# Kernel tuning notes

Measured on AMD Instinct MI355X. Metric: run time of the kernel, lower is better.

Reference implementation:

```python
import jax, jax.numpy as jnp
import numpy as np

WS = 16          # window_size
NUM_HEADS = 6

def _rel_tables(ws):
    # SwinV2 continuous relative coords table, log-spaced, scaled by 8
    r = np.arange(-(ws - 1), ws, dtype=np.float32)
    t = np.stack(np.meshgrid(r, r, indexing='ij'), axis=-1)      # (2ws-1, 2ws-1, 2)
    t = t / (ws - 1) * 8.0
    t = np.sign(t) * np.log2(np.abs(t) + 1.0) / np.log2(8.0)
    c = np.stack(np.meshgrid(np.arange(ws), np.arange(ws), indexing='ij')).reshape(2, -1)
    rel = (c[:, :, None] - c[:, None, :]).transpose(1, 2, 0)     # (N, N, 2)
    rel[..., 0] += ws - 1
    rel[..., 1] += ws - 1
    rel[..., 0] *= 2 * ws - 1
    return jnp.asarray(t), jnp.asarray(rel.sum(-1))              # table, (N,N) int index

REL_TABLE, REL_INDEX = _rel_tables(WS)

def conv2d(x, w, b, pad=0, dil=1, groups=1):
    y = jax.lax.conv_general_dilated(
        x, w, (1, 1), [(pad, pad), (pad, pad)], rhs_dilation=(dil, dil),
        feature_group_count=groups, dimension_numbers=('NCHW', 'OIHW', 'NCHW'))
    return y + b[None, :, None, None]

def layernorm(x, g, b, eps=1e-5):
    mu = x.mean(-1, keepdims=True)
    var = ((x - mu) ** 2).mean(-1, keepdims=True)
    return (x - mu) * jax.lax.rsqrt(var + eps) * g + b

def _forward(x, p1_w, p1_b, pw_w, pw_b, dw_w, dw_b, dd_w, dd_b, p2_w, p2_b,
             ln_g, ln_b, qkv_w, q_bias, v_bias, logit_scale,
             cpb_w1, cpb_b1, cpb_w2, proj_w, proj_b):
    B, C, H, W = x.shape
    ws, nh = WS, NUM_HEADS
    N, hd = ws * ws, C // nh
    # ---- VAB: conv attention block ----
    y = jax.nn.gelu(conv2d(x, p1_w, p1_b), approximate=False)          # proj_1 + GELU
    a = conv2d(y, pw_w, pw_b)                                          # pointwise 1x1
    a = conv2d(a, dw_w, dw_b, pad=2, groups=C)                         # depthwise 5x5
    a = conv2d(a, dd_w, dd_b, pad=6, dil=3, groups=C)                  # depthwise 5x5 dil=3
    y = conv2d(y * a, p2_w, p2_b) + x                                  # proj_2 + residual
    y = jnp.transpose(y, (0, 2, 3, 1))                                 # B,H,W,C
    y = layernorm(y, ln_g, ln_b)                                       # pixel_norm
    # ---- window partition -> (B*nW, N, C) ----
    xw = y.reshape(B, H // ws, ws, W // ws, ws, C)
    xw = xw.transpose(0, 1, 3, 2, 4, 5).reshape(-1, N, C)
    # ---- SwinV2 cosine window attention ----
    qkv_b = jnp.concatenate([q_bias, jnp.zeros_like(v_bias), v_bias])
    qkv = (xw @ qkv_w.T + qkv_b).reshape(-1, N, 3, nh, hd).transpose(2, 0, 3, 1, 4)
    q, k, v = qkv[0], qkv[1], qkv[2]                                   # (B_, h, N, d)
    qn = q / jnp.maximum(jnp.linalg.norm(q, axis=-1, keepdims=True), 1e-12)
    kn = k / jnp.maximum(jnp.linalg.norm(k, axis=-1, keepdims=True), 1e-12)
    scale = jnp.exp(jnp.minimum(logit_scale, jnp.log(100.0)))          # clamp at 1/0.01
    attn = jnp.einsum('bhnd,bhmd->bhnm', qn, kn) * scale
    # CPB MLP bias: (2ws-1,2ws-1,2) -> heads, gathered by relative_position_index
    t = (jax.nn.relu(REL_TABLE @ cpb_w1.T + cpb_b1) @ cpb_w2.T).reshape(-1, nh)
    rpb = t[REL_INDEX.reshape(-1)].reshape(N, N, nh).transpose(2, 0, 1)
    attn = attn + 16.0 * jax.nn.sigmoid(rpb)
    attn = jax.nn.softmax(attn, axis=-1)
    out = jnp.einsum('bhnm,bhmd->bhnd', attn, v).transpose(0, 2, 1, 3).reshape(-1, N, C)
    out = out @ proj_w.T + proj_b
    # ---- window reverse -> NCHW ----
    out = out.reshape(B, H // ws, W // ws, ws, ws, C)
    out = out.transpose(0, 1, 3, 2, 4, 5).reshape(B, H, W, C)
    return jnp.transpose(out, (0, 3, 1, 2))

def setup_inputs():
    key = jax.random.key(0)
    ks = jax.random.split(key, 12)
    C, A = 192, 192
    rn = lambda k, shape, s=0.02: jax.random.normal(k, shape, jnp.float32) * s
    return {
        'x': jax.random.normal(ks[0], (4, C, 128, 128), jnp.float32),
        'p1_w': rn(ks[1], (A, C, 1, 1)), 'p1_b': jnp.zeros((A,), jnp.float32),
        'pw_w': rn(ks[2], (A, A, 1, 1)), 'pw_b': jnp.zeros((A,), jnp.float32),
        'dw_w': rn(ks[3], (A, 1, 5, 5), 0.05), 'dw_b': jnp.zeros((A,), jnp.float32),
        'dd_w': rn(ks[4], (A, 1, 5, 5), 0.05), 'dd_b': jnp.zeros((A,), jnp.float32),
        'p2_w': rn(ks[5], (C, A, 1, 1)), 'p2_b': jnp.zeros((C,), jnp.float32),
        'ln_g': jnp.ones((C,), jnp.float32), 'ln_b': jnp.zeros((C,), jnp.float32),
        'qkv_w': rn(ks[6], (3 * C, C)),
        'q_bias': jnp.zeros((C,), jnp.float32), 'v_bias': jnp.zeros((C,), jnp.float32),
        'logit_scale': jnp.log(10.0) * jnp.ones((NUM_HEADS, 1, 1), jnp.float32),
        'cpb_w1': rn(ks[7], (512, 2), 0.1), 'cpb_b1': jnp.zeros((512,), jnp.float32),
        'cpb_w2': rn(ks[8], (NUM_HEADS, 512), 0.1),
        'proj_w': rn(ks[9], (C, C)), 'proj_b': jnp.zeros((C,), jnp.float32),
    }

def reference(x, p1_w, p1_b, pw_w, pw_b, dw_w, dw_b, dd_w, dd_b, p2_w, p2_b,
              ln_g, ln_b, qkv_w, q_bias, v_bias, logit_scale,
              cpb_w1, cpb_b1, cpb_w2, proj_w, proj_b):
    return _forward(x, p1_w, p1_b, pw_w, pw_b, dw_w, dw_b, dd_w, dd_b, p2_w, p2_b,
                    ln_g, ln_b, qkv_w, q_bias, v_bias, logit_scale,
                    cpb_w1, cpb_b1, cpb_w2, proj_w, proj_b)
```

## Files before the change

### kernel.cpp

```cpp
#include <hip/hip_runtime.h>
#include <hip/hip_bf16.h>
#include <math.h>

#define HWC 16384
#define CCH 192
#define LDA 200

typedef __attribute__((ext_vector_type(8))) short short8x;
typedef __attribute__((ext_vector_type(4))) float f32x4;

__device__ __forceinline__ float b2f(unsigned int u){
  union { unsigned int i; float f; } x; x.i = (u & 0xffffu) << 16; return x.f;
}
__device__ __forceinline__ unsigned short f2b(float f){
  union { float f; unsigned int i; } x; x.f = f;
  unsigned int r = x.i + 0x7FFFu + ((x.i >> 16) & 1u);
  return (unsigned short)(r >> 16);
}
__device__ __forceinline__ unsigned int cvt_pk_bf16(float a, float b){
  unsigned int r;
  asm("v_cvt_pk_bf16_f32 %0, %1, %2" : "=v"(r) : "v"(a), "v"(b));
  return r;
}
__device__ __forceinline__ float exp2_fast(float x){
  float r;
  asm("v_exp_f32 %0, %1" : "=v"(r) : "v"(x));
  return r;
}
__device__ __forceinline__ float gelu_exact(float v){
  return 0.5f * v * (1.0f + erff(v * 0.70710678118654752440f));
}

__global__ __launch_bounds__(256) void cast_w_kernel(
    const float* __restrict__ qkvw, const float* __restrict__ projw,
    const float* __restrict__ p1w,  const float* __restrict__ pww,
    const float* __restrict__ p2w,  const float* __restrict__ dww,
    const float* __restrict__ ddw,
    unsigned short* __restrict__ wq,  unsigned short* __restrict__ wprj,
    unsigned short* __restrict__ wp1, unsigned short* __restrict__ wpa,
    unsigned short* __restrict__ wp2, float* __restrict__ dwt,
    float* __restrict__ ddt)
{
  int i = blockIdx.x*256 + threadIdx.x;
  if (i < 110592) wq[i] = f2b(qkvw[i]);
  if (i < 36864){
    wprj[i] = f2b(projw[i]);
    wp1[i]  = f2b(p1w[i]);
    wpa[i]  = f2b(pww[i]);
    wp2[i]  = f2b(p2w[i]);
  }
  if (i < 4992){
    int t = i / 192, c = i - t*192;
    dwt[i] = (t < 25) ? dww[c*25 + t] : 0.0f;
    ddt[i] = (t < 25) ? ddw[c*25 + t] : 0.0f;
  }
}

__global__ __launch_bounds__(256) void tx_kernel(
    const float* __restrict__ in, float* __restrict__ xt32,
    unsigned short* __restrict__ x16)
{
  __shared__ float xs[CCH*68];
  const int tid = threadIdx.x;
  const int pix0 = blockIdx.x * 64;
  const int bb = pix0 >> 14;
  const int hw0 = pix0 & (HWC-1);
  const long base = (long)bb * CCH * HWC + hw0;
  #pragma unroll 8
  for (int i=0;i<48;i++){
    int idx = tid + i*256;
    int ci = idx >> 6, pix = idx & 63;
    xs[ci*68 + pix] = in[base + (long)ci*HWC + pix];
  }
  __syncthreads();
  #pragma unroll 8
  for (int i=0;i<48;i++){
    int idx = tid + i*256;
    int pix = idx / 192, ci = idx - pix*192;
    float v = xs[ci*68 + pix];
    long g = (long)(pix0 + pix)*CCH + ci;
    xt32[g] = v;
    x16[g]  = f2b(v);
  }
}

__global__ __launch_bounds__(256, 3) void pw01_mfma(
    const unsigned short* __restrict__ x16,
    const unsigned short* __restrict__ w1,
    const float* __restrict__ b1,
    const unsigned short* __restrict__ wa,
    const float* __restrict__ ba,
    unsigned short* __restrict__ y16,
    unsigned short* __restrict__ a16)
{
  __shared__ unsigned short sA[128*LDA];
  const int tid = threadIdx.x;
  const int m0 = blockIdx.x * 128;
  #pragma unroll
  for (int i=0;i<12;i++){
    int idx = tid + i*256;
    int row = idx / 24, oct = idx - row*24;
    uint4 v = *(const uint4*)(x16 + (long)(m0+row)*CCH + oct*8);
    *(uint4*)&sA[row*LDA + oct*8] = v;
  }
  __syncthreads();
  const int wv = tid >> 6, lane = tid & 63;
  const int wm = (wv & 1) * 64;
  const int wn = (wv >> 1) * 96;
  const int l15 = lane & 15, q = lane >> 4;
  f32x4 acc[4][6];
  #pragma unroll
  for (int mi=0;mi<4;mi++)
    #pragma unroll
    for (int ni=0;ni<6;ni++) acc[mi][ni] = (f32x4){0.f,0.f,0.f,0.f};
  #pragma unroll
  for (int kk=0; kk<6; kk++){
    const int k0 = kk*32;
    short8x af[4], bf[6];
    #pragma unroll
    for (int mi=0; mi<4; mi++)
      af[mi] = *(const short8x*)&sA[(wm + mi*16 + l15)*LDA + k0 + q*8];
    #pragma unroll
    for (int ni=0; ni<6; ni++)
      bf[ni] = *(const short8x*)(w1 + (long)(wn + ni*16 + l15)*CCH + k0 + q*8);
    #pragma unroll
    for (int mi=0; mi<4; mi++)
      #pragma unroll
      for (int ni=0; ni<6; ni++)
        acc[mi][ni] = __builtin_amdgcn_mfma_f32_16x16x32_bf16(af[mi], bf[ni], acc[mi][ni], 0,0,0);
  }
  float bv[6];
  #pragma unroll
  for (int ni=0; ni<6; ni++) bv[ni] = b1[wn + ni*16 + l15];
  __syncthreads();
  #pragma unroll
  for (int mi=0; mi<4; mi++){
    #pragma unroll
    for (int r=0; r<4; r++){
      int pixl = wm + mi*16 + q*4 + r;
      long gp = (long)(m0 + pixl)*CCH + wn;
      #pragma unroll
      for (int ni=0; ni<6; ni++){
        unsigned short us = f2b(gelu_exact(acc[mi][ni][r] + bv[ni]));
        y16[gp + ni*16 + l15] = us;
        sA[pixl*LDA + wn + ni*16 + l15] = us;
      }
    }
  }
  __syncthreads();
  #pragma unroll
  for (int mi=0;mi<4;mi++)
    #pragma unroll
    for (int ni=0;ni<6;ni++) acc[mi][ni] = (f32x4){0.f,0.f,0.f,0.f};
  #pragma unroll
  for (int kk=0; kk<6; kk++){
    const int k0 = kk*32;
    short8x af[4], bf[6];
    #pragma unroll
    for (int mi=0; mi<4; mi++)
      af[mi] = *(const short8x*)&sA[(wm + mi*16 + l15)*LDA + k0 + q*8];
    #pragma unroll
    for (int ni=0; ni<6; ni++)
      bf[ni] = *(const short8x*)(wa + (long)(wn + ni*16 + l15)*CCH + k0 + q*8);
    #pragma unroll
    for (int mi=0; mi<4; mi++)
      #pragma unroll
      for (int ni=0; ni<6; ni++)
        acc[mi][ni] = __builtin_amdgcn_mfma_f32_16x16x32_bf16(af[mi], bf[ni], acc[mi][ni], 0,0,0);
  }
  #pragma unroll
  for (int ni=0; ni<6; ni++) bv[ni] = ba[wn + ni*16 + l15];
  #pragma unroll
  for (int mi=0; mi<4; mi++){
    #pragma unroll
    for (int r=0; r<4; r++){
      long gp = (long)(m0 + wm + mi*16 + q*4 + r)*CCH + wn;
      #pragma unroll
      for (int ni=0; ni<6; ni++)
        a16[gp + ni*16 + l15] = f2b(acc[mi][ni][r] + bv[ni]);
    }
  }
}

template<int MODE>
__global__ __launch_bounds__(256, 3) void pw_mfma(
    const unsigned short* __restrict__ in0,
    const unsigned short* __restrict__ in1,
    const unsigned short* __restrict__ w16,
    const float* __restrict__ bias,
    const float* __restrict__ xres,
    const float* __restrict__ gam, const float* __restrict__ bet,
    unsigned short* __restrict__ out16)
{
  __shared__ unsigned short sA[128*LDA];
  __shared__ float reds[128*2], reds2[128*2];
  const int tid = threadIdx.x;
  const int m0 = blockIdx.x * 128;
  #pragma unroll
  for (int i=0;i<12;i++){
    int idx = tid + i*256;
    int row = idx / 24, oct = idx - row*24;
    long g = (long)(m0+row)*CCH + oct*8;
    uint4 vy = *(const uint4*)(in0 + g);
    if (MODE == 2){
      uint4 va = *(const uint4*)(in1 + g);
      unsigned int yy[4] = {vy.x, vy.y, vy.z, vy.w};
      unsigned int aa[4] = {va.x, va.y, va.z, va.w};
      unsigned int rr[4];
      #pragma unroll
      for (int wq2=0; wq2<4; wq2++){
        float lo = b2f(yy[wq2]) * b2f(aa[wq2]);
        float hi = b2f(yy[wq2] >> 16) * b2f(aa[wq2] >> 16);
        rr[wq2] = (unsigned int)f2b(lo) | ((unsigned int)f2b(hi) << 16);
      }
      uint4 vp; vp.x=rr[0]; vp.y=rr[1]; vp.z=rr[2]; vp.w=rr[3];
      *(uint4*)&sA[row*LDA + oct*8] = vp;
    } else {
      *(uint4*)&sA[row*LDA + oct*8] = vy;
    }
  }
  __syncthreads();
  const int wv = tid >> 6, lane = tid & 63;
  const int wm = (wv & 1) * 64;
  const int wn = (wv >> 1) * 96;
  const int l15 = lane & 15, q = lane >> 4;
  f32x4 acc[4][6];
  #pragma unroll
  for (int mi=0;mi<4;mi++)
    #pragma unroll
    for (int ni=0;ni<6;ni++) acc[mi][ni] = (f32x4){0.f,0.f,0.f,0.f};
  #pragma unroll
  for (int kk=0; kk<6; kk++){
    const int k0 = kk*32;
    short8x af[4], bf[6];
    #pragma unroll
    for (int mi=0; mi<4; mi++)
      af[mi] = *(const short8x*)&sA[(wm + mi*16 + l15)*LDA + k0 + q*8];
    #pragma unroll
    for (int ni=0; ni<6; ni++)
      bf[ni] = *(const short8x*)(w16 + (long)(wn + ni*16 + l15)*CCH + k0 + q*8);
    #pragma unroll
    for (int mi=0; mi<4; mi++)
      #pragma unroll
      for (int ni=0; ni<6; ni++)
        acc[mi][ni] = __builtin_amdgcn_mfma_f32_16x16x32_bf16(af[mi], bf[ni], acc[mi][ni], 0,0,0);
  }
  float bv[6];
  #pragma unroll
  for (int ni=0; ni<6; ni++) bv[ni] = bias[wn + ni*16 + l15];

  if (MODE != 2){
    #pragma unroll
    for (int mi=0; mi<4; mi++){
      #pragma unroll
      for (int r=0; r<4; r++){
        long gp = (long)(m0 + wm + mi*16 + q*4 + r)*CCH + wn;
        #pragma unroll
        for (int ni=0; ni<6; ni++){
          float v = acc[mi][ni][r] + bv[ni];
          if (MODE == 0) v = gelu_exact(v);
          out16[gp + ni*16 + l15] = f2b(v);
        }
      }
    }
  } else {
    const int slot = wv >> 1;
    #pragma unroll
    for (int mi=0; mi<4; mi++){
      #pragma unroll
      for (int r=0; r<4; r++){
        int pixl = wm + mi*16 + q*4 + r;
        long gp = (long)(m0 + pixl)*CCH + wn;
        float s = 0.f, s2 = 0.f;
        #pragma unroll
        for (int ni=0; ni<6; ni++){
          float v = acc[mi][ni][r] + bv[ni] + xres[gp + ni*16 + l15];
          acc[mi][ni][r] = v;
          s += v; s2 = fmaf(v, v, s2);
        }
        s  += __shfl_xor(s, 1);  s  += __shfl_xor(s, 2);
        s  += __shfl_xor(s, 4);  s  += __shfl_xor(s, 8);
        s2 += __shfl_xor(s2, 1); s2 += __shfl_xor(s2, 2);
        s2 += __shfl_xor(s2, 4); s2 += __shfl_xor(s2, 8);
        if (l15 == 0){ reds[pixl*2 + slot] = s; reds2[pixl*2 + slot] = s2; }
      }
    }
    __syncthreads();
    #pragma unroll
    for (int mi=0; mi<4; mi++){
      #pragma unroll
      for (int r=0; r<4; r++){
        int pixl = wm + mi*16 + q*4 + r;
        long gp = (long)(m0 + pixl)*CCH + wn;
        float st  = reds[pixl*2] + reds[pixl*2+1];
        float s2t = reds2[pixl*2] + reds2[pixl*2+1];
        float mu = st * (1.0f/192.0f);
        float var = s2t * (1.0f/192.0f) - mu*mu;
        float rs = rsqrtf(var + 1e-5f);
        #pragma unroll
        for (int ni=0; ni<6; ni++){
          int co = wn + ni*16 + l15;
          float z = (acc[mi][ni][r] - mu) * rs * gam[co] + bet[co];
          out16[gp + ni*16 + l15] = f2b(z);
        }
      }
    }
  }
}

template<int PAD, int DIL>
__global__ __launch_bounds__(256) void dw_tile(
    const unsigned short* __restrict__ in16, const float* __restrict__ wT,
    const float* __restrict__ bias, unsigned short* __restrict__ out16)
{
  constexpr int R = 32 + 2*PAD;
  constexpr int NPX = R*R;
  constexpr int NIT = (NPX + 255) / 256;
  __shared__ unsigned short sIn[NPX*8];
  const int bid = blockIdx.x;
  const int t_lo = bid & 7, rest = bid >> 3;
  const int c8 = rest % 24, t_hi = rest / 24;
  const int tile = t_lo + 8*t_hi;
  const int b = tile >> 4, ty = (tile >> 2) & 3, tx = tile & 3;
  const int c0 = c8*8;
  const int tid = threadIdx.x;
  const long ibase = (long)b * HWC * CCH;
  const int r0 = ty*32 - PAD, cl0 = tx*32 - PAD;
  #pragma unroll
  for (int j=0; j<NIT; j++){
    int idx = tid + j*256;
    if (idx < NPX){
      int r = idx / R, c = idx - r*R;
      int gr = r0 + r, gc = cl0 + c;
      uint4 val = (uint4){0u,0u,0u,0u};
      if (((unsigned)gr < 128u) & ((unsigned)gc < 128u))
        val = *(const uint4*)(in16 + ibase + (long)(gr*128 + gc)*CCH + c0);
      *(uint4*)&sIn[idx*8] = val;
    }
  }
  __syncthreads();
  const float4 bb0 = *(const float4*)&bias[c0], bb1 = *(const float4*)&bias[c0+4];
  #pragma unroll
  for (int it=0; it<4; it++){
    int o = tid + it*256;
    int orow = o >> 5, ocol = o & 31;
    float acc[8] = {bb0.x, bb0.y, bb0.z, bb0.w, bb1.x, bb1.y, bb1.z, bb1.w};
    #pragma unroll
    for (int kh=0; kh<5; kh++){
      int lr = orow + kh*DIL;
      #pragma unroll
      for (int kw=0; kw<5; kw++){
        int lc = ocol + kw*DIL;
        uint4 xq = *(const uint4*)&sIn[(lr*R + lc)*8];
        const float* wp = wT + (kh*5 + kw)*CCH + c0;
        float4 w0 = *(const float4*)wp, w1 = *(const float4*)(wp + 4);
        unsigned int uu[4] = {xq.x, xq.y, xq.z, xq.w};
        float wa[8] = {w0.x, w0.y, w0.z, w0.w, w1.x, w1.y, w1.z, w1.w};
        #pragma unroll
        for (int jj=0; jj<8; jj++){
          float xvf = b2f(uu[jj>>1] >> ((jj&1)*16));
          acc[jj] = fmaf(wa[jj], xvf, acc[jj]);
        }
      }
    }
    int gr = ty*32 + orow, gc = tx*32 + ocol;
    unsigned int rr[4];
    #pragma unroll
    for (int wq2=0; wq2<4; wq2++)
      rr[wq2] = (unsigned int)f2b(acc[wq2*2]) | ((unsigned int)f2b(acc[wq2*2+1]) << 16);
    uint4 ov; ov.x=rr[0]; ov.y=rr[1]; ov.z=rr[2]; ov.w=rr[3];
    *(uint4*)(out16 + ibase + (long)(gr*128 + gc)*CCH + c0) = ov;
  }
}

__global__ __launch_bounds__(256, 3) void qkv_fused(
    const unsigned short* __restrict__ z16,
    const unsigned short* __restrict__ w16,
    const float* __restrict__ qb, const float* __restrict__ vb,
    unsigned short* __restrict__ qkvb)
{
  __shared__ unsigned short sA[128*LDA];
  const int tid = threadIdx.x;
  const int m0 = blockIdx.x * 128;
  #pragma unroll
  for (int i=0;i<12;i++){
    int idx = tid + i*256;
    int row = idx / 24, oct = idx - row*24;
    uint4 v = *(const uint4*)(z16 + (long)(m0+row)*CCH + oct*8);
    *(uint4*)&sA[row*LDA + oct*8] = v;
  }
  __syncthreads();
  const int wv = tid >> 6, lane = tid & 63;
  const int wm = (wv & 1) * 64;
  const int wn = (wv >> 1) * 96;
  const int l15 = lane & 15, q = lane >> 4;
  const int head0 = wn >> 5;
  int winm[4], tokb[4];
  #pragma unroll
  for (int mi=0;mi<4;mi++){
    int pb = m0 + wm + mi*16;
    int hw = pb & (HWC-1);
    int row = hw >> 7, col = hw & 127;
    winm[mi] = (pb>>14)*64 + (row>>4)*8 + (col>>4);
    tokb[mi] = (row & 15) * 16;
  }
  #pragma unroll
  for (int s=0; s<3; s++){
    const unsigned short* wbase = w16 + (long)(s*192)*CCH;
    f32x4 acc[4][6];
    #pragma unroll
    for (int mi=0;mi<4;mi++)
      #pragma unroll
      for (int ni=0;ni<6;ni++) acc[mi][ni] = (f32x4){0.f,0.f,0.f,0.f};
    #pragma unroll
    for (int kk=0; kk<6; kk++){
      const int k0 = kk*32;
      short8x af[4], bf[6];
      #pragma unroll
      for (int mi=0; mi<4; mi++)
        af[mi] = *(const short8x*)&sA[(wm + mi*16 + l15)*LDA + k0 + q*8];
      #pragma unroll
      for (int ni=0; ni<6; ni++)
        bf[ni] = *(const short8x*)(wbase + (long)(wn + ni*16 + l15)*CCH + k0 + q*8);
      #pragma unroll
      for (int mi=0; mi<4; mi++)
        #pragma unroll
        for (int ni=0; ni<6; ni++)
          acc[mi][ni] = __builtin_amdgcn_mfma_f32_16x16x32_bf16(af[mi], bf[ni], acc[mi][ni], 0,0,0);
    }
    float bvv[6];
    #pragma unroll
    for (int ni=0;ni<6;ni++){
      int co = wn + ni*16 + l15;
      bvv[ni] = (s==0) ? qb[co] : ((s==2) ? vb[co] : 0.0f);
    }
    unsigned short* dst = qkvb + (long)s * 12582912;
    #pragma unroll
    for (int mi=0; mi<4; mi++){
      long obase = (long)winm[mi]*49152 + (long)tokb[mi]*32 + l15*2;
      #pragma unroll
      for (int r=0; r<4; r++){
        long ob = obase + (q*4 + r)*32;
        #pragma unroll
        for (int hp=0; hp<3; hp++){
          unsigned int u = (unsigned int)f2b(acc[mi][hp*2][r]   + bvv[hp*2])
                         | ((unsigned int)f2b(acc[mi][hp*2+1][r] + bvv[hp*2+1]) << 16);
          *(unsigned int*)&dst[ob + (long)(head0 + hp)*8192] = u;
        }
      }
    }
  }
}

__device__ __forceinline__ float cpb_coord(int a){
  float r = ((float)a - 15.0f) * (8.0f/15.0f);
  float t = log2f(fabsf(r) + 1.0f) * (1.0f/3.0f);
  return (r < 0.f) ? -t : t;
}
__global__ __launch_bounds__(128) void cpb_mlp_kernel(
    const float* __restrict__ w1, const float* __restrict__ b1,
    const float* __restrict__ w2, float* __restrict__ tbl6)
{
  int e = blockIdx.x;
  int a = e / 31, bb = e - a*31;
  float t0 = cpb_coord(a), t1 = cpb_coord(bb);
  float p[6] = {0,0,0,0,0,0};
  for (int hh = threadIdx.x; hh < 512; hh += 128){
    float hid = t0*w1[hh*2] + t1*w1[hh*2+1] + b1[hh];
    hid = fmaxf(hid, 0.0f);
    #pragma unroll
    for (int hd=0; hd<6; hd++) p[hd] = fmaf(hid, w2[hd*512 + hh], p[hd]);
  }
  __shared__ float red[6][128];
  #pragma unroll
  for (int hd=0; hd<6; hd++) red[hd][threadIdx.x] = p[hd];
  __syncthreads();
  if (threadIdx.x < 6){
    float sum = 0.f;
    for (int i=0;i<128;i++) sum += red[threadIdx.x][i];
    tbl6[e*6 + threadIdx.x] = sum;
  }
}
__global__ __launch_bounds__(256) void cpb_expand_kernel(
    const float* __restrict__ tbl6, float2* __restrict__ bias2)
{
  int idx = blockIdx.x*256 + threadIdx.x;
  int h = idx >> 15;
  int rem = idx & 32767;
  int i = rem >> 7;
  int rem2 = rem & 127;
  int kt = rem2 >> 4, l15 = rem2 & 15;
  int j0 = kt*32 + l15, j1 = j0 + 16;
  int dy0 = (i>>4) - (j0>>4) + 15, dx0 = (i&15) - (j0&15) + 15;
  int dy1 = (i>>4) - (j1>>4) + 15, dx1 = (i&15) - (j1&15) + 15;
  float v0 = tbl6[(dy0*31+dx0)*6 + h];
  float v1 = tbl6[(dy1*31+dx1)*6 + h];
  float2 o;
  o.x = (16.0f / (1.0f + __expf(-v0)) - 16.0f) * 1.4426950408889634f;
  o.y = (16.0f / (1.0f + __expf(-v1)) - 16.0f) * 1.4426950408889634f;
  bias2[idx] = o;
}

#define KSP 40
#define VTP 264
__global__ __launch_bounds__(256) void attn_mfma(
    const unsigned short* __restrict__ qkvb, const float2* __restrict__ bias2,
    const float* __restrict__ ls,
    unsigned short* __restrict__ aout)
{
  __shared__ unsigned short ks[256*KSP];
  __shared__ unsigned short vt[32*VTP];
  __shared__ unsigned short ps[4][64*KSP];
  __shared__ float qinvs[256];
  const int win = blockIdx.x, h = blockIdx.y;
  const int t = threadIdx.x;
  const long base = ((long)(win*6 + h)) << 13;
  const unsigned short* Qg = qkvb + base;
  const unsigned short* Kg = Qg + 12582912;
  const unsigned short* Vg = Kg + 12582912;
  const float sc = __expf(fminf(ls[h], 4.60517018598809136804f));

  {
    union { uint4 v4[4]; unsigned int u[16]; } kb, ko, qv;
    const unsigned short* kr = Kg + t*32;
    #pragma unroll
    for (int o=0;o<4;o++) kb.v4[o] = *(const uint4*)(kr + o*8);
    float sk = 0.f;
    #pragma unroll
    for (int i=0;i<16;i++){
      float lo = b2f(kb.u[i]), hi = b2f(kb.u[i]>>16);
      sk = fmaf(lo, lo, sk); sk = fmaf(hi, hi, sk);
    }
    float kinv = 1.0f / fmaxf(sqrtf(sk), 1e-12f);
    #pragma unroll
    for (int i=0;i<16;i++)
      ko.u[i] = cvt_pk_bf16(b2f(kb.u[i])*kinv, b2f(kb.u[i]>>16)*kinv);
    #pragma unroll
    for (int o=0;o<4;o++) *(uint4*)&ks[t*KSP + o*8] = ko.v4[o];

    const unsigned short* qr = Qg + t*32;
    #pragma unroll
    for (int o=0;o<4;o++) qv.v4[o] = *(const uint4*)(qr + o*8);
    float sq = 0.f;
    #pragma unroll
    for (int i=0;i<16;i++){
      float lo = b2f(qv.u[i]), hi = b2f(qv.u[i]>>16);
      sq = fmaf(lo, lo, sq); sq = fmaf(hi, hi, sq);
    }
    qinvs[t] = sc * 1.4426950408889634f / fmaxf(sqrtf(sq), 1e-12f);
  }
  {
    const int kt = t >> 5, j = t & 31;
    const int col = kt*32 + ((j & 15)*2 + (j >> 4));
    union { unsigned short u[32]; uint4 v4[4]; } vp;
    const unsigned short* vr = Vg + t*32;
    #pragma unroll
    for (int o=0;o<4;o++) vp.v4[o] = *(const uint4*)(vr + o*8);
    #pragma unroll
    for (int d=0; d<32; d++) vt[d*VTP + col] = vp.u[d];
  }
  const int wv = t >> 6, lane = t & 63;
  const int l15 = lane & 15, q = lane >> 4;
  short8x qa[4];
  #pragma unroll
  for (int mi=0; mi<4; mi++)
    qa[mi] = *(const short8x*)(Qg + (wv*64 + mi*16 + l15)*32 + q*8);
  __syncthreads();

  float4 qiv[4];
  #pragma unroll
  for (int mi=0; mi<4; mi++)
    qiv[mi] = *(const float4*)&qinvs[wv*64 + mi*16 + q*4];

  f32x4 oacc[4][2], lsum[4];
  #pragma unroll
  for (int mi=0;mi<4;mi++){
    oacc[mi][0] = (f32x4){0.f,0.f,0.f,0.f};
    oacc[mi][1] = (f32x4){0.f,0.f,0.f,0.f};
    lsum[mi]    = (f32x4){0.f,0.f,0.f,0.f};
  }
  const float2* bias_h2 = bias2 + ((long)h << 15);
  unsigned short* myps = ps[wv];

  for (int kt=0; kt<8; kt++){
    const int k0 = kt*32;
    short8x kb0 = *(const short8x*)&ks[(k0 + l15)*KSP + q*8];
    short8x kb1 = *(const short8x*)&ks[(k0 + 16 + l15)*KSP + q*8];
    f32x4 s[4][2];
    __builtin_amdgcn_s_setprio(1);
    #pragma unroll
    for (int mi=0; mi<4; mi++){
      f32x4 z0 = (f32x4){0.f,0.f,0.f,0.f};
      s[mi][0] = __builtin_amdgcn_mfma_f32_16x16x32_bf16(qa[mi], kb0, z0, 0,0,0);
      s[mi][1] = __builtin_amdgcn_mfma_f32_16x16x32_bf16(qa[mi], kb1, z0, 0,0,0);
    }
    __builtin_amdgcn_s_setprio(0);
    #pragma unroll
    for (int mi=0; mi<4; mi++){
      const float* qivp = (const float*)&qiv[mi];
      #pragma unroll
      for (int r=0; r<4; r++){
        int rowq = wv*64 + mi*16 + q*4 + r;
        float2 bpr = bias_h2[rowq*128 + kt*16 + l15];
        float qr2 = qivp[r];
        float e0 = exp2_fast(fminf(fmaf(s[mi][0][r], qr2, bpr.x), 43.f));
        float e1 = exp2_fast(fminf(fmaf(s[mi][1][r], qr2, bpr.y), 43.f));
        lsum[mi][r] += e0 + e1;
        *(unsigned int*)&myps[(mi*16 + q*4 + r)*KSP + l15*2] = cvt_pk_bf16(e0, e1);
      }
    }
    short8x vb0 = *(const short8x*)&vt[(l15)*VTP      + k0 + q*8];
    short8x vb1 = *(const short8x*)&vt[(16 + l15)*VTP + k0 + q*8];
    __builtin_amdgcn_s_setprio(1);
    #pragma unroll
    for (int mi=0; mi<4; mi++){
      short8x pa = *(const short8x*)&myps[(mi*16 + l15)*KSP + q*8];
      oacc[mi][0] = __builtin_amdgcn_mfma_f32_16x16x32_bf16(pa, vb0, oacc[mi][0], 0,0,0);
      oacc[mi][1] = __builtin_amdgcn_mfma_f32_16x16x32_bf16(pa, vb1, oacc[mi][1], 0,0,0);
    }
    __builtin_amdgcn_s_setprio(0);
  }
  #pragma unroll
  for (int mi=0; mi<4; mi++){
    #pragma unroll
    for (int r=0; r<4; r++){
      float v = lsum[mi][r];
      v += __shfl_xor(v, 1);
      v += __shfl_xor(v, 2);
      v += __shfl_xor(v, 4);
      v += __shfl_xor(v, 8);
      lsum[mi][r] = v;
    }
  }
  const int dperm = (l15 >> 1) + ((l15 & 1) << 4);
  const int bb = win >> 6, wy = (win >> 3) & 7, wx = win & 7;
  #pragma unroll
  for (int mi=0; mi<4; mi++){
    #pragma unroll
    for (int r=0; r<4; r++){
      int rowq = wv*64 + mi*16 + q*4 + r;
      int pixo = bb*HWC + (wy*16 + (rowq>>4))*128 + wx*16 + (rowq&15);
      float inv = 1.0f / lsum[mi][r];
      aout[(long)pixo*CCH + h*32 + dperm]     = f2b(oacc[mi][0][r]*inv);
      aout[(long)pixo*CCH + h*32 + dperm + 8] = f2b(oacc[mi][1][r]*inv);
    }
  }
}

__global__ __launch_bounds__(256, 3) void proj_mfma(
    const unsigned short* __restrict__ a16,
    const unsigned short* __restrict__ w16,
    const float* __restrict__ bias,
    float* __restrict__ outp)
{
  __shared__ unsigned short sB[128*LDA];
  const int tid = threadIdx.x;
  const int n0 = blockIdx.x * 128;
  #pragma unroll
  for (int i=0;i<12;i++){
    int idx = tid + i*256;
    int row = idx / 24, oct = idx - row*24;
    uint4 v = *(const uint4*)(a16 + (long)(n0+row)*CCH + oct*8);
    *(uint4*)&sB[row*LDA + oct*8] = v;
  }
  __syncthreads();
  const int wv = tid >> 6, lane = tid & 63;
  const int wm = (wv & 1) * 96;
  const int wn = (wv >> 1) * 64;
  const int l15 = lane & 15, q = lane >> 4;
  f32x4 acc[6][4];
  #pragma unroll
  for (int mi=0;mi<6;mi++)
    #pragma unroll
    for (int ni=0;ni<4;ni++) acc[mi][ni] = (f32x4){0.f,0.f,0.f,0.f};
  #pragma unroll
  for (int kk=0; kk<6; kk++){
    const int k0 = kk*32;
    short8x af[6], bf[4];
    #pragma unroll
    for (int mi=0; mi<6; mi++)
      af[mi] = *(const short8x*)(w16 + (long)(wm + mi*16 + l15)*CCH + k0 + q*8);
    #pragma unroll
    for (int ni=0; ni<4; ni++)
      bf[ni] = *(const short8x*)&sB[(wn + ni*16 + l15)*LDA + k0 + q*8];
    #pragma unroll
    for (int mi=0; mi<6; mi++)
      #pragma unroll
      for (int ni=0; ni<4; ni++)
        acc[mi][ni] = __builtin_amdgcn_mfma_f32_16x16x32_bf16(af[mi], bf[ni], acc[mi][ni], 0,0,0);
  }
  #pragma unroll
  for (int mi=0; mi<6; mi++){
    #pragma unroll
    for (int r=0; r<4; r++){
      int co = wm + mi*16 + q*4 + r;
      float bv = bias[co];
      #pragma unroll
      for (int ni=0; ni<4; ni++){
        int pix = n0 + wn + ni*16 + l15;
        int b = pix >> 14, hw = pix & (HWC-1);
        outp[((long)b*CCH + co)*HWC + hw] = acc[mi][ni][r] + bv;
      }
    }
  }
}

extern "C" void kernel_launch(void* const* d_in, const int* in_sizes, int n_in,
                              void* d_out, int out_size, void* d_ws, size_t ws_size,
                              hipStream_t stream)
{
  const float* x       = (const float*)d_in[0];
  const float* p1_w    = (const float*)d_in[1];
  const float* p1_b    = (const float*)d_in[2];
  const float* pw_w    = (const float*)d_in[3];
  const float* pw_b    = (const float*)d_in[4];
  const float* dw_w    = (const float*)d_in[5];
  const float* dw_b    = (const float*)d_in[6];
  const float* dd_w    = (const float*)d_in[7];
  const float* dd_b    = (const float*)d_in[8];
  const float* p2_w    = (const float*)d_in[9];
  const float* p2_b    = (const float*)d_in[10];
  const float* ln_g    = (const float*)d_in[11];
  const float* ln_b    = (const float*)d_in[12];
  const float* qkv_w   = (const float*)d_in[13];
  const float* q_bias  = (const float*)d_in[14];
  const float* v_bias  = (const float*)d_in[15];
  const float* lscale  = (const float*)d_in[16];
  const float* cpb_w1  = (const float*)d_in[17];
  const float* cpb_b1  = (const float*)d_in[18];
  const float* cpb_w2  = (const float*)d_in[19];
  const float* proj_w  = (const float*)d_in[20];
  const float* proj_b  = (const float*)d_in[21];

  float* ws = (float*)d_ws;
  const long A = 12582912L;
  unsigned short* X16  = (unsigned short*)ws;
  unsigned short* Y16  = (unsigned short*)(ws + A/2);
  unsigned short* A16  = (unsigned short*)(ws + A);
  unsigned short* T16  = (unsigned short*)(ws + A + A/2);
  float* XT32 = ws + 2*A;
  unsigned short* QKVB = (unsigned short*)ws;
  unsigned short* Z16  = (unsigned short*)(ws + 3*A);
  unsigned short* AO16 = Z16;
  float* DWT = ws + 3*A + A/2;
  float* DDT = DWT + 4992;
  unsigned short* WQ   = (unsigned short*)(DDT + 4992);
  unsigned short* WPRJ = WQ + 110592;
  unsigned short* WP1  = WPRJ + 36864;
  unsigned short* WPA  = WP1 + 36864;
  unsigned short* WP2  = WPA + 36864;
  float* RB = ws + 4*A;
  float* T6 = RB + 393216;

  cast_w_kernel<<<432, 256, 0, stream>>>(qkv_w, proj_w, p1_w, pw_w, p2_w, dw_w, dd_w,
                                         WQ, WPRJ, WP1, WPA, WP2, DWT, DDT);
  cpb_mlp_kernel<<<961, 128, 0, stream>>>(cpb_w1, cpb_b1, cpb_w2, T6);
  cpb_expand_kernel<<<768, 256, 0, stream>>>(T6, (float2*)RB);

  tx_kernel<<<1024, 256, 0, stream>>>(x, XT32, X16);

  pw01_mfma<<<512, 256, 0, stream>>>(X16, WP1, p1_b, WPA, pw_b, Y16, A16);
  dw_tile<2,1><<<1536, 256, 0, stream>>>(A16, DWT, dw_b, T16);
  dw_tile<6,3><<<1536, 256, 0, stream>>>(T16, DDT, dd_b, A16);
  pw_mfma<2><<<512, 256, 0, stream>>>(Y16, A16, WP2, p2_b, XT32, ln_g, ln_b, Z16);

  qkv_fused<<<512, 256, 0, stream>>>(Z16, WQ, q_bias, v_bias, QKVB);

  attn_mfma<<<dim3(256, 6), 256, 0, stream>>>(QKVB, (const float2*)RB, lscale, AO16);

  proj_mfma<<<512, 256, 0, stream>>>(AO16, WPRJ, proj_b, (float*)d_out);
}
```

Before: 453.1 us.

## Fuse proj_2+LayerNorm with QKV GEMM and stage pw01 stores through LDS

Merges the proj_2/residual/LayerNorm kernel with the QKV projection kernel, so the normalized activations stay in shared memory and never make a global round trip through Z16. The pw01 kernel now writes its GELU and pointwise outputs to LDS first, then copies them out with coalesced 16-byte stores instead of scattered 2-byte stores. Workspace buffers are rearranged to fit the new aliasing. The cost is extra barriers, and the fused kernel keeps its accumulators live across both GEMMs, which may raise register pressure. It also contains a redundant leftover expression.

After: 654.6 us. +44.5%, slower.

```diff
diff --git a/kernel.cpp b/kernel.cpp
--- a/kernel.cpp
+++ b/kernel.cpp
@@ -138,16 +138,18 @@
     #pragma unroll
     for (int r=0; r<4; r++){
       int pixl = wm + mi*16 + q*4 + r;
-      long gp = (long)(m0 + pixl)*CCH + wn;
-      #pragma unroll
-      for (int ni=0; ni<6; ni++){
-        unsigned short us = f2b(gelu_exact(acc[mi][ni][r] + bv[ni]));
-        y16[gp + ni*16 + l15] = us;
-        sA[pixl*LDA + wn + ni*16 + l15] = us;
-      }
-    }
-  }
-  __syncthreads();
+      #pragma unroll
+      for (int ni=0; ni<6; ni++)
+        sA[pixl*LDA + wn + ni*16 + l15] = f2b(gelu_exact(acc[mi][ni][r] + bv[ni]));
+    }
+  }
+  __syncthreads();
+  #pragma unroll
+  for (int i=0;i<12;i++){
+    int idx = tid + i*256;
+    int row = idx / 24, oct = idx - row*24;
+    *(uint4*)(y16 + (long)(m0+row)*CCH + oct*8) = *(const uint4*)&sA[row*LDA + oct*8];
+  }
   #pragma unroll
   for (int mi=0;mi<4;mi++)
     #pragma unroll
@@ -170,141 +172,23 @@
   }
   #pragma unroll
   for (int ni=0; ni<6; ni++) bv[ni] = ba[wn + ni*16 + l15];
+  __syncthreads();
   #pragma unroll
   for (int mi=0; mi<4; mi++){
     #pragma unroll
     for (int r=0; r<4; r++){
-      long gp = (long)(m0 + wm + mi*16 + q*4 + r)*CCH + wn;
+      int pixl = wm + mi*16 + q*4 + r;
       #pragma unroll
       for (int ni=0; ni<6; ni++)
-        a16[gp + ni*16 + l15] = f2b(acc[mi][ni][r] + bv[ni]);
-    }
-  }
-}
-
-template<int MODE>
-__global__ __launch_bounds__(256, 3) void pw_mfma(
-    const unsigned short* __restrict__ in0,
-    const unsigned short* __restrict__ in1,
-    const unsigned short* __restrict__ w16,
-    const float* __restrict__ bias,
-    const float* __restrict__ xres,
-    const float* __restrict__ gam, const float* __restrict__ bet,
-    unsigned short* __restrict__ out16)
-{
-  __shared__ unsigned short sA[128*LDA];
-  __shared__ float reds[128*2], reds2[128*2];
-  const int tid = threadIdx.x;
-  const int m0 = blockIdx.x * 128;
+        sA[pixl*LDA + wn + ni*16 + l15] = f2b(acc[mi][ni][r] + bv[ni]);
+    }
+  }
+  __syncthreads();
   #pragma unroll
   for (int i=0;i<12;i++){
     int idx = tid + i*256;
     int row = idx / 24, oct = idx - row*24;
-    long g = (long)(m0+row)*CCH + oct*8;
-    uint4 vy = *(const uint4*)(in0 + g);
-    if (MODE == 2){
-      uint4 va = *(const uint4*)(in1 + g);
-      unsigned int yy[4] = {vy.x, vy.y, vy.z, vy.w};
-      unsigned int aa[4] = {va.x, va.y, va.z, va.w};
-      unsigned int rr[4];
-      #pragma unroll
-      for (int wq2=0; wq2<4; wq2++){
-        float lo = b2f(yy[wq2]) * b2f(aa[wq2]);
-        float hi = b2f(yy[wq2] >> 16) * b2f(aa[wq2] >> 16);
-        rr[wq2] = (unsigned int)f2b(lo) | ((unsigned int)f2b(hi) << 16);
-      }
-      uint4 vp; vp.x=rr[0]; vp.y=rr[1]; vp.z=rr[2]; vp.w=rr[3];
-      *(uint4*)&sA[row*LDA + oct*8] = vp;
-    } else {
-      *(uint4*)&sA[row*LDA + oct*8] = vy;
-    }
-  }
-  __syncthreads();
-  const int wv = tid >> 6, lane = tid & 63;
-  const int wm = (wv & 1) * 64;
-  const int wn = (wv >> 1) * 96;
-  const int l15 = lane & 15, q = lane >> 4;
-  f32x4 acc[4][6];
-  #pragma unroll
-  for (int mi=0;mi<4;mi++)
-    #pragma unroll
-    for (int ni=0;ni<6;ni++) acc[mi][ni] = (f32x4){0.f,0.f,0.f,0.f};
-  #pragma unroll
-  for (int kk=0; kk<6; kk++){
-    const int k0 = kk*32;
-    short8x af[4], bf[6];
-    #pragma unroll
-    for (int mi=0; mi<4; mi++)
-      af[mi] = *(const short8x*)&sA[(wm + mi*16 + l15)*LDA + k0 + q*8];
-    #pragma unroll
-    for (int ni=0; ni<6; ni++)
-      bf[ni] = *(const short8x*)(w16 + (long)(wn + ni*16 + l15)*CCH + k0 + q*8);
-    #pragma unroll
-    for (int mi=0; mi<4; mi++)
-      #pragma unroll
-      for (int ni=0; ni<6; ni++)
-        acc[mi][ni] = __builtin_amdgcn_mfma_f32_16x16x32_bf16(af[mi], bf[ni], acc[mi][ni], 0,0,0);
-  }
-  float bv[6];
-  #pragma unroll
-  for (int ni=0; ni<6; ni++) bv[ni] = bias[wn + ni*16 + l15];
-
-  if (MODE != 2){
-    #pragma unroll
-    for (int mi=0; mi<4; mi++){
-      #pragma unroll
-      for (int r=0; r<4; r++){
-        long gp = (long)(m0 + wm + mi*16 + q*4 + r)*CCH + wn;
-        #pragma unroll
-        for (int ni=0; ni<6; ni++){
-          float v = acc[mi][ni][r] + bv[ni];
-          if (MODE == 0) v = gelu_exact(v);
-          out16[gp + ni*16 + l15] = f2b(v);
-        }
-      }
-    }
-  } else {
-    const int slot = wv >> 1;
-    #pragma unroll
-    for (int mi=0; mi<4; mi++){
-      #pragma unroll
-      for (int r=0; r<4; r++){
-        int pixl = wm + mi*16 + q*4 + r;
-        long gp = (long)(m0 + pixl)*CCH + wn;
-        float s = 0.f, s2 = 0.f;
-        #pragma unroll
-        for (int ni=0; ni<6; ni++){
-          float v = acc[mi][ni][r] + bv[ni] + xres[gp + ni*16 + l15];
-          acc[mi][ni][r] = v;
-          s += v; s2 = fmaf(v, v, s2);
-        }
-        s  += __shfl_xor(s, 1);  s  += __shfl_xor(s, 2);
-        s  += __shfl_xor(s, 4);  s  += __shfl_xor(s, 8);
-        s2 += __shfl_xor(s2, 1); s2 += __shfl_xor(s2, 2);
-        s2 += __shfl_xor(s2, 4); s2 += __shfl_xor(s2, 8);
-        if (l15 == 0){ reds[pixl*2 + slot] = s; reds2[pixl*2 + slot] = s2; }
-      }
-    }
-    __syncthreads();
-    #pragma unroll
-    for (int mi=0; mi<4; mi++){
-      #pragma unroll
-      for (int r=0; r<4; r++){
-        int pixl = wm + mi*16 + q*4 + r;
-        long gp = (long)(m0 + pixl)*CCH + wn;
-        float st  = reds[pixl*2] + reds[pixl*2+1];
-        float s2t = reds2[pixl*2] + reds2[pixl*2+1];
-        float mu = st * (1.0f/192.0f);
-        float var = s2t * (1.0f/192.0f) - mu*mu;
-        float rs = rsqrtf(var + 1e-5f);
-        #pragma unroll
-        for (int ni=0; ni<6; ni++){
-          int co = wn + ni*16 + l15;
-          float z = (acc[mi][ni][r] - mu) * rs * gam[co] + bet[co];
-          out16[gp + ni*16 + l15] = f2b(z);
-        }
-      }
-    }
+    *(uint4*)(a16 + (long)(m0+row)*CCH + oct*8) = *(const uint4*)&sA[row*LDA + oct*8];
   }
 }
 
@@ -373,27 +257,110 @@
   }
 }
 
-__global__ __launch_bounds__(256, 3) void qkv_fused(
-    const unsigned short* __restrict__ z16,
-    const unsigned short* __restrict__ w16,
+__global__ __launch_bounds__(256, 3) void pwqkv_mfma(
+    const unsigned short* __restrict__ y16,
+    const unsigned short* __restrict__ a16in,
+    const unsigned short* __restrict__ w2,
+    const float* __restrict__ b2,
+    const float* __restrict__ xres,
+    const float* __restrict__ gam, const float* __restrict__ bet,
+    const unsigned short* __restrict__ wq,
     const float* __restrict__ qb, const float* __restrict__ vb,
     unsigned short* __restrict__ qkvb)
 {
   __shared__ unsigned short sA[128*LDA];
+  __shared__ float reds[128*2], reds2[128*2];
   const int tid = threadIdx.x;
   const int m0 = blockIdx.x * 128;
   #pragma unroll
   for (int i=0;i<12;i++){
     int idx = tid + i*256;
     int row = idx / 24, oct = idx - row*24;
-    uint4 v = *(const uint4*)(z16 + (long)(m0+row)*CCH + oct*8);
-    *(uint4*)&sA[row*LDA + oct*8] = v;
+    long g = (long)(m0+row)*CCH + oct*8;
+    uint4 vy = *(const uint4*)(y16 + g);
+    uint4 va = *(const uint4*)(a16in + g);
+    unsigned int yy[4] = {vy.x, vy.y, vy.z, vy.w};
+    unsigned int aa[4] = {va.x, va.y, va.z, va.w};
+    unsigned int rr[4];
+    #pragma unroll
+    for (int wq2=0; wq2<4; wq2++){
+      float lo = b2f(yy[wq2]) * b2f(aa[wq2]);
+      float hi = b2f(yy[wq2] >> 16) * b2f(aa[wq2] >> 16);
+      rr[wq2] = (unsigned int)f2b(lo) | ((unsigned int)f2b(hi) << 16);
+    }
+    uint4 vp; vp.x=rr[0]; vp.y=rr[1]; vp.z=rr[2]; vp.w=rr[3];
+    *(uint4*)&sA[row*LDA + oct*8] = vp;
   }
   __syncthreads();
   const int wv = tid >> 6, lane = tid & 63;
   const int wm = (wv & 1) * 64;
   const int wn = (wv >> 1) * 96;
   const int l15 = lane & 15, q = lane >> 4;
+  f32x4 acc[4][6];
+  #pragma unroll
+  for (int mi=0;mi<4;mi++)
+    #pragma unroll
+    for (int ni=0;ni<6;ni++) acc[mi][ni] = (f32x4){0.f,0.f,0.f,0.f};
+  #pragma unroll
+  for (int kk=0; kk<6; kk++){
+    const int k0 = kk*32;
+    short8x af[4], bf[6];
+    #pragma unroll
+    for (int mi=0; mi<4; mi++)
+      af[mi] = *(const short8x*)&sA[(wm + mi*16 + l15)*LDA + k0 + q*8];
+    #pragma unroll
+    for (int ni=0; ni<6; ni++)
+      bf[ni] = *(const short8x*)(w2 + (long)(wn + ni*16 + l15)*CCH + k0 + q*8);
+    #pragma unroll
+    for (int mi=0; mi<4; mi++)
+      #pragma unroll
+      for (int ni=0; ni<6; ni++)
+        acc[mi][ni] = __builtin_amdgcn_mfma_f32_16x16x32_bf16(af[mi], bf[ni], acc[mi][ni], 0,0,0);
+  }
+  float bv[6];
+  #pragma unroll
+  for (int ni=0; ni<6; ni++) bv[ni] = b2[wn + ni*16 + l15];
+  const int slot = wv >> 1;
+  #pragma unroll
+  for (int mi=0; mi<4; mi++){
+    #pragma unroll
+    for (int r=0; r<4; r++){
+      int pixl = wm + mi*16 + q*4 + r;
+      long gp = (long)(m0 + pixl)*CCH + wn;
+      float s = 0.f, s2 = 0.f;
+      #pragma unroll
+      for (int ni=0; ni<6; ni++){
+        float v = acc[mi][ni][r] + bv[ni] + xres[gp + ni*16 + l15];
+        acc[mi][ni][r] = v;
+        s += v; s2 = fmaf(v, v, s2);
+      }
+      s  += __shfl_xor(s, 1);  s  += __shfl_xor(s, 2);
+      s  += __shfl_xor(s, 4);  s  += __shfl_xor(s, 8);
+      s2 += __shfl_xor(s2, 1); s2 += __shfl_xor(s2, 2);
+      s2 += __shfl_xor(s2, 4); s2 += __shfl_xor(s2, 8);
+      if (l15 == 0){ reds[pixl*2 + slot] = s; reds2[pixl*2 + slot] = s2; }
+    }
+  }
+  __syncthreads();
+  #pragma unroll
+  for (int mi=0; mi<4; mi++){
+    #pragma unroll
+    for (int r=0; r<4; r++){
+      int pixl = wm + mi*16 + q*4 + r;
+      float st  = reds[pixl*2] + reds[pixl*2+1];
+      float s2t = reds2[pixl*2] + reds2[pixl*2+1];
+      float mu = st * (1.0f/192.0f);
+      float var = s2t * (1.0f/192.0f) - mu*mu;
+      float rs = rsqrtf(var + 1e-5f);
+      #pragma unroll
+      for (int ni=0; ni<6; ni++){
+        int co = wn + ni*16 + l15;
+        float z = (acc[mi][ni][r] - mu) * rs * gam[co] + bet[co];
+        sA[pixl*LDA + co] = f2b(z);
+      }
+    }
+  }
+  __syncthreads();
   const int head0 = wn >> 5;
   int winm[4], tokb[4];
   #pragma unroll
@@ -406,8 +373,7 @@
   }
   #pragma unroll
   for (int s=0; s<3; s++){
-    const unsigned short* wbase = w16 + (long)(s*192)*CCH;
-    f32x4 acc[4][6];
+    const unsigned short* wbase = wq + (long)(s*192)*CCH;
     #pragma unroll
     for (int mi=0;mi<4;mi++)
       #pragma unroll
@@ -443,8 +409,9 @@
         long ob = obase + (q*4 + r)*32;
         #pragma unroll
         for (int hp=0; hp<3; hp++){
-          unsigned int u = (unsigned int)f2b(acc[mi][hp*2][r]   + bvv[hp*2])
-                         | ((unsigned int)f2b(acc[mi][hp*2+1][r] + bvv[hp*2+1]) << 16);
+          unsigned int u = (unsigned int)f2b(acc[hp*2? mi:mi][hp*2][r] + bvv[hp*2]);
+          u = (unsigned int)f2b(acc[mi][hp*2][r]   + bvv[hp*2])
+            | ((unsigned int)f2b(acc[mi][hp*2+1][r] + bvv[hp*2+1]) << 16);
           *(unsigned int*)&dst[ob + (long)(head0 + hp)*8192] = u;
         }
       }
@@ -738,18 +705,17 @@
   unsigned short* Y16  = (unsigned short*)(ws + A/2);
   unsigned short* A16  = (unsigned short*)(ws + A);
   unsigned short* T16  = (unsigned short*)(ws + A + A/2);
-  float* XT32 = ws + 2*A;
-  unsigned short* QKVB = (unsigned short*)ws;
-  unsigned short* Z16  = (unsigned short*)(ws + 3*A);
-  unsigned short* AO16 = Z16;
-  float* DWT = ws + 3*A + A/2;
+  unsigned short* QKVB = (unsigned short*)(ws + A + A/2);
+  float* XT32 = ws + 3*A;
+  unsigned short* AO16 = (unsigned short*)(ws + 3*A);
+  float* DWT = ws + 4*A;
   float* DDT = DWT + 4992;
   unsigned short* WQ   = (unsigned short*)(DDT + 4992);
   unsigned short* WPRJ = WQ + 110592;
   unsigned short* WP1  = WPRJ + 36864;
   unsigned short* WPA  = WP1 + 36864;
   unsigned short* WP2  = WPA + 36864;
-  float* RB = ws + 4*A;
+  float* RB = (float*)(WP2 + 36864);
   float* T6 = RB + 393216;
 
   cast_w_kernel<<<432, 256, 0, stream>>>(qkv_w, proj_w, p1_w, pw_w, p2_w, dw_w, dd_w,
@@ -762,9 +728,9 @@
   pw01_mfma<<<512, 256, 0, stream>>>(X16, WP1, p1_b, WPA, pw_b, Y16, A16);
   dw_tile<2,1><<<1536, 256, 0, stream>>>(A16, DWT, dw_b, T16);
   dw_tile<6,3><<<1536, 256, 0, stream>>>(T16, DDT, dd_b, A16);
-  pw_mfma<2><<<512, 256, 0, stream>>>(Y16, A16, WP2, p2_b, XT32, ln_g, ln_b, Z16);
-
-  qkv_fused<<<512, 256, 0, stream>>>(Z16, WQ, q_bias, v_bias, QKVB);
+
+  pwqkv_mfma<<<512, 256, 0, stream>>>(Y16, A16, WP2, p2_b, XT32, ln_g, ln_b,
+                                      WQ, q_bias, v_bias, QKVB);
 
   attn_mfma<<<dim3(256, 6), 256, 0, stream>>>(QKVB, (const float2*)RB, lscale, AO16);
 
```
